# Optimization experiments

Measured on AMD Instinct MI355X. Metric: run time of the kernel, lower is better.

Reference implementation:

```python
import jax, jax.numpy as jnp
import numpy as np

N_NODES = 100000
N_EDGES = 1600000
N_GRAPHS = 256
NODE = 64
EDGE = 64
GLOB = 64
HID = 64


def _lin_init(key, fan_in, fan_out):
    kw, kb = jax.random.split(key)
    bound = 1.0 / np.sqrt(fan_in)
    W = jax.random.uniform(kw, (fan_in, fan_out), minval=-bound, maxval=bound, dtype=jnp.float32)
    b = jax.random.uniform(kb, (fan_out,), minval=-bound, maxval=bound, dtype=jnp.float32)
    return W, b


def setup_inputs() -> dict:
    key = jax.random.key(0)
    ks = jax.random.split(key, 9)
    x = jax.random.normal(ks[0], (N_NODES, NODE), dtype=jnp.float32)
    edge_index = jax.random.randint(ks[1], (2, N_EDGES), 0, N_NODES, dtype=jnp.int32)
    edge_attr = jax.random.normal(ks[2], (N_EDGES, EDGE), dtype=jnp.float32)
    u = jax.random.normal(ks[3], (N_GRAPHS, GLOB), dtype=jnp.float32)
    batch = jnp.sort(jax.random.randint(ks[4], (N_NODES,), 0, N_GRAPHS, dtype=jnp.int32))
    W1a, b1a = _lin_init(ks[5], NODE + EDGE, HID)
    W1b, b1b = _lin_init(ks[6], HID, HID)
    W2a, b2a = _lin_init(ks[7], NODE + HID + GLOB, HID)
    W2b, b2b = _lin_init(ks[8], HID, NODE)
    return {"x": x, "edge_index": edge_index, "edge_attr": edge_attr, "u": u,
            "batch": batch, "W1a": W1a, "b1a": b1a, "W1b": W1b, "b1b": b1b,
            "W2a": W2a, "b2a": b2a, "W2b": W2b, "b2b": b2b}


def reference(x, edge_index, edge_attr, u, batch, W1a, b1a, W1b, b1b, W2a, b2a, W2b, b2b):
    row, col = edge_index[0], edge_index[1]
    # gather source node feats + edge feats -> [E, node+edge]
    out = jnp.concatenate([x[row], edge_attr], axis=1)
    out = jax.nn.selu(out @ W1a + b1a) @ W1b + b1b  # node_mlp_1 -> [E, HID]
    # scatter_mean into destination nodes
    summed = jax.ops.segment_sum(out, col, num_segments=x.shape[0])
    counts = jax.ops.segment_sum(jnp.ones((out.shape[0],), out.dtype), col, num_segments=x.shape[0])
    mean = summed / jnp.maximum(counts, 1.0)[:, None]
    h = jnp.concatenate([x, mean, u[batch]], axis=1)  # [N, node+HID+glob]
    return jax.nn.selu(h @ W2a + b2a) @ W2b + b2b
```

## Files before the change

### kernel.cpp

```cpp
#include <hip/hip_runtime.h>

#define NN 100000
#define NE 1600000

typedef __attribute__((ext_vector_type(8))) short short8;
typedef __attribute__((ext_vector_type(4))) float f32x4;

__device__ __forceinline__ short f2b(float x) {
    unsigned u = __builtin_bit_cast(unsigned, x);
    u = (u + 0x7FFFu + ((u >> 16) & 1u)) >> 16;
    return (short)u;
}

__device__ __forceinline__ float selu_f(float x) {
    const float scale = 1.0507009873554805f;
    const float asc   = 1.7580993408473766f;
    return x > 0.f ? scale * x : asc * (__expf(x) - 1.f);
}

__device__ __forceinline__ short8 pack8(const float* __restrict__ p) {
    const float4 a = *reinterpret_cast<const float4*>(p);
    const float4 b = *reinterpret_cast<const float4*>(p + 4);
    short8 r;
    r[0] = f2b(a.x); r[1] = f2b(a.y); r[2] = f2b(a.z); r[3] = f2b(a.w);
    r[4] = f2b(b.x); r[5] = f2b(b.y); r[6] = f2b(b.z); r[7] = f2b(b.w);
    return r;
}

__device__ __forceinline__ short8 pack8s(const float* __restrict__ p, float s) {
    const float4 a = *reinterpret_cast<const float4*>(p);
    const float4 b = *reinterpret_cast<const float4*>(p + 4);
    short8 r;
    r[0] = f2b(a.x * s); r[1] = f2b(a.y * s); r[2] = f2b(a.z * s); r[3] = f2b(a.w * s);
    r[4] = f2b(b.x * s); r[5] = f2b(b.y * s); r[6] = f2b(b.z * s); r[7] = f2b(b.w * s);
    return r;
}

__device__ __forceinline__ short8 wfrag(const float* __restrict__ W, int t, int n, int p, int q) {
    const float* base = W + (t * 32 + q * 8) * 64 + n * 16 + p;
    short8 r;
#pragma unroll
    for (int j = 0; j < 8; ++j) r[j] = f2b(base[j * 64]);
    return r;
}

__device__ __forceinline__ f32x4 mm(short8 a, short8 b, f32x4 c) {
    return __builtin_amdgcn_mfma_f32_16x16x32_bf16(a, b, c, 0, 0, 0);
}

__global__ __launch_bounds__(256) void edge_kernel(
    const float* __restrict__ x, const int* __restrict__ row, const int* __restrict__ col,
    const float* __restrict__ ea,
    const float* __restrict__ W1a, const float* __restrict__ b1a,
    const float* __restrict__ W1b, const float* __restrict__ b1b,
    float* __restrict__ summed, float* __restrict__ counts)
{
    __shared__ __attribute__((aligned(16))) short hlds[4][16 * 72];
    const int lane = threadIdx.x & 63;
    const int wid  = threadIdx.x >> 6;
    const int p = lane & 15, q = lane >> 4;
    short* hl = hlds[wid];

    short8 B1[4][4], B2[2][4];
#pragma unroll
    for (int t = 0; t < 4; ++t)
#pragma unroll
        for (int n = 0; n < 4; ++n) B1[t][n] = wfrag(W1a, t, n, p, q);
#pragma unroll
    for (int t = 0; t < 2; ++t)
#pragma unroll
        for (int n = 0; n < 4; ++n) B2[t][n] = wfrag(W1b, t, n, p, q);
    float bias1[4], bias2[4];
#pragma unroll
    for (int n = 0; n < 4; ++n) { bias1[n] = b1a[n * 16 + p]; bias2[n] = b1b[n * 16 + p]; }

    const int nwave = gridDim.x * 4;
    for (int tile = blockIdx.x * 4 + wid; tile < NE / 16; tile += nwave) {
        const int e  = tile * 16 + p;
        const int rs = row[e];
        const float* xr = x + rs * 64 + q * 8;
        const float* er = ea + e * 64 + q * 8;
        short8 a0 = pack8(xr);
        short8 a1 = pack8(xr + 32);
        short8 a2 = pack8(er);
        short8 a3 = pack8(er + 32);

        f32x4 acc[4];
#pragma unroll
        for (int n = 0; n < 4; ++n) acc[n] = (f32x4){0.f, 0.f, 0.f, 0.f};
#pragma unroll
        for (int n = 0; n < 4; ++n) {
            acc[n] = mm(a0, B1[0][n], acc[n]);
            acc[n] = mm(a1, B1[1][n], acc[n]);
            acc[n] = mm(a2, B1[2][n], acc[n]);
            acc[n] = mm(a3, B1[3][n], acc[n]);
        }
#pragma unroll
        for (int n = 0; n < 4; ++n)
#pragma unroll
            for (int i = 0; i < 4; ++i)
                hl[(q * 4 + i) * 72 + n * 16 + p] = f2b(selu_f(acc[n][i] + bias1[n]));

        short8 h0 = *reinterpret_cast<const short8*>(hl + p * 72 + q * 8);
        short8 h1 = *reinterpret_cast<const short8*>(hl + p * 72 + 32 + q * 8);

        f32x4 acc2[4];
#pragma unroll
        for (int n = 0; n < 4; ++n) acc2[n] = (f32x4){0.f, 0.f, 0.f, 0.f};
#pragma unroll
        for (int n = 0; n < 4; ++n) {
            acc2[n] = mm(h0, B2[0][n], acc2[n]);
            acc2[n] = mm(h1, B2[1][n], acc2[n]);
        }

        int cd[4];
#pragma unroll
        for (int i = 0; i < 4; ++i) cd[i] = col[tile * 16 + q * 4 + i];
#pragma unroll
        for (int n = 0; n < 4; ++n)
#pragma unroll
            for (int i = 0; i < 4; ++i)
                unsafeAtomicAdd(&summed[cd[i] * 64 + n * 16 + p], acc2[n][i] + bias2[n]);
        if (lane < 16) unsafeAtomicAdd(&counts[col[e]], 1.0f);
    }
}

__global__ __launch_bounds__(256) void node_kernel(
    const float* __restrict__ x, const float* __restrict__ u, const int* __restrict__ batch,
    const float* __restrict__ summed, const float* __restrict__ counts,
    const float* __restrict__ W2a, const float* __restrict__ b2a,
    const float* __restrict__ W2b, const float* __restrict__ b2b,
    float* __restrict__ out)
{
    __shared__ __attribute__((aligned(16))) short hlds[4][16 * 72];
    const int lane = threadIdx.x & 63;
    const int wid  = threadIdx.x >> 6;
    const int p = lane & 15, q = lane >> 4;
    short* hl = hlds[wid];

    short8 BA[6][4], BB[2][4];
#pragma unroll
    for (int t = 0; t < 6; ++t)
#pragma unroll
        for (int n = 0; n < 4; ++n) BA[t][n] = wfrag(W2a, t, n, p, q);
#pragma unroll
    for (int t = 0; t < 2; ++t)
#pragma unroll
        for (int n = 0; n < 4; ++n) BB[t][n] = wfrag(W2b, t, n, p, q);
    float bias1[4], bias2[4];
#pragma unroll
    for (int n = 0; n < 4; ++n) { bias1[n] = b2a[n * 16 + p]; bias2[n] = b2b[n * 16 + p]; }

    const int nwave = gridDim.x * 4;
    for (int tile = blockIdx.x * 4 + wid; tile < NN / 16; tile += nwave) {
        const int v = tile * 16 + p;
        const float* xr = x + v * 64 + q * 8;
        short8 a0 = pack8(xr);
        short8 a1 = pack8(xr + 32);
        const float rc = 1.f / fmaxf(counts[v], 1.f);
        const float* sr = summed + v * 64 + q * 8;
        short8 a2 = pack8s(sr, rc);
        short8 a3 = pack8s(sr + 32, rc);
        const int g = batch[v];
        const float* ur = u + g * 64 + q * 8;
        short8 a4 = pack8(ur);
        short8 a5 = pack8(ur + 32);

        f32x4 acc[4];
#pragma unroll
        for (int n = 0; n < 4; ++n) acc[n] = (f32x4){0.f, 0.f, 0.f, 0.f};
#pragma unroll
        for (int n = 0; n < 4; ++n) {
            acc[n] = mm(a0, BA[0][n], acc[n]);
            acc[n] = mm(a1, BA[1][n], acc[n]);
            acc[n] = mm(a2, BA[2][n], acc[n]);
            acc[n] = mm(a3, BA[3][n], acc[n]);
            acc[n] = mm(a4, BA[4][n], acc[n]);
            acc[n] = mm(a5, BA[5][n], acc[n]);
        }
#pragma unroll
        for (int n = 0; n < 4; ++n)
#pragma unroll
            for (int i = 0; i < 4; ++i)
                hl[(q * 4 + i) * 72 + n * 16 + p] = f2b(selu_f(acc[n][i] + bias1[n]));

        short8 h0 = *reinterpret_cast<const short8*>(hl + p * 72 + q * 8);
        short8 h1 = *reinterpret_cast<const short8*>(hl + p * 72 + 32 + q * 8);

        f32x4 acc2[4];
#pragma unroll
        for (int n = 0; n < 4; ++n) acc2[n] = (f32x4){0.f, 0.f, 0.f, 0.f};
#pragma unroll
        for (int n = 0; n < 4; ++n) {
            acc2[n] = mm(h0, BB[0][n], acc2[n]);
            acc2[n] = mm(h1, BB[1][n], acc2[n]);
        }
#pragma unroll
        for (int n = 0; n < 4; ++n)
#pragma unroll
            for (int i = 0; i < 4; ++i)
                out[(tile * 16 + q * 4 + i) * 64 + n * 16 + p] = acc2[n][i] + bias2[n];
    }
}

extern "C" void kernel_launch(void* const* d_in, const int* in_sizes, int n_in,
                              void* d_out, int out_size, void* d_ws, size_t ws_size,
                              hipStream_t stream) {
    const float* x     = (const float*)d_in[0];
    const int*   ei    = (const int*)d_in[1];
    const float* ea    = (const float*)d_in[2];
    const float* u     = (const float*)d_in[3];
    const int*   batch = (const int*)d_in[4];
    const float* W1a   = (const float*)d_in[5];
    const float* b1a   = (const float*)d_in[6];
    const float* W1b   = (const float*)d_in[7];
    const float* b1b   = (const float*)d_in[8];
    const float* W2a   = (const float*)d_in[9];
    const float* b2a   = (const float*)d_in[10];
    const float* W2b   = (const float*)d_in[11];
    const float* b2b   = (const float*)d_in[12];
    float* out = (float*)d_out;

    float* summed = (float*)d_ws;
    float* counts = summed + (size_t)NN * 64;

    hipMemsetAsync(d_ws, 0, ((size_t)NN * 64 + NN) * sizeof(float), stream);

    const int* row = ei;
    const int* col = ei + NE;
    edge_kernel<<<1024, 256, 0, stream>>>(x, row, col, ea, W1a, b1a, W1b, b1b, summed, counts);
    node_kernel<<<512, 256, 0, stream>>>(x, u, batch, summed, counts, W2a, b2a, W2b, b2b, out);
}
```

Baseline: 882.5 us.

## Accumulate edge scatter in bf16 with packed atomics and prepack weight fragments

Stores the per-node sum buffer as bf16 and scatters edge messages with global_atomic_pk_add_bf16, pairing neighbouring lanes through a shuffle. This halves atomic traffic and the size of the buffer to clear. Weight fragments are converted to bf16 MFMA layout once by a small setup kernel instead of strided per-wave loads. The change also prefetches the next row index, uses nontemporal loads for edge_attr and doubles the node kernel grid. Summing up to many bf16 additions per node loses precision and may exceed tolerance.

```diff
diff --git a/kernel.cpp b/kernel.cpp
--- a/kernel.cpp
+++ b/kernel.cpp
@@ -2,6 +2,8 @@
 
 #define NN 100000
 #define NE 1600000
+#define NT_E (NE / 16)
+#define NT_N ((NN + 15) / 16)
 
 typedef __attribute__((ext_vector_type(8))) short short8;
 typedef __attribute__((ext_vector_type(4))) float f32x4;
@@ -11,6 +13,9 @@
     u = (u + 0x7FFFu + ((u >> 16) & 1u)) >> 16;
     return (short)u;
 }
+__device__ __forceinline__ float b2f(unsigned short b) {
+    return __builtin_bit_cast(float, (unsigned)b << 16);
+}
 
 __device__ __forceinline__ float selu_f(float x) {
     const float scale = 1.0507009873554805f;
@@ -19,41 +24,55 @@
 }
 
 __device__ __forceinline__ short8 pack8(const float* __restrict__ p) {
-    const float4 a = *reinterpret_cast<const float4*>(p);
-    const float4 b = *reinterpret_cast<const float4*>(p + 4);
+    const f32x4 a = *reinterpret_cast<const f32x4*>(p);
+    const f32x4 b = *reinterpret_cast<const f32x4*>(p + 4);
     short8 r;
-    r[0] = f2b(a.x); r[1] = f2b(a.y); r[2] = f2b(a.z); r[3] = f2b(a.w);
-    r[4] = f2b(b.x); r[5] = f2b(b.y); r[6] = f2b(b.z); r[7] = f2b(b.w);
+#pragma unroll
+    for (int j = 0; j < 4; ++j) { r[j] = f2b(a[j]); r[j + 4] = f2b(b[j]); }
     return r;
 }
 
-__device__ __forceinline__ short8 pack8s(const float* __restrict__ p, float s) {
-    const float4 a = *reinterpret_cast<const float4*>(p);
-    const float4 b = *reinterpret_cast<const float4*>(p + 4);
+__device__ __forceinline__ short8 pack8nt(const float* __restrict__ p) {
+    const f32x4 a = __builtin_nontemporal_load(reinterpret_cast<const f32x4*>(p));
+    const f32x4 b = __builtin_nontemporal_load(reinterpret_cast<const f32x4*>(p + 4));
     short8 r;
-    r[0] = f2b(a.x * s); r[1] = f2b(a.y * s); r[2] = f2b(a.z * s); r[3] = f2b(a.w * s);
-    r[4] = f2b(b.x * s); r[5] = f2b(b.y * s); r[6] = f2b(b.z * s); r[7] = f2b(b.w * s);
+#pragma unroll
+    for (int j = 0; j < 4; ++j) { r[j] = f2b(a[j]); r[j + 4] = f2b(b[j]); }
     return r;
 }
 
-__device__ __forceinline__ short8 wfrag(const float* __restrict__ W, int t, int n, int p, int q) {
-    const float* base = W + (t * 32 + q * 8) * 64 + n * 16 + p;
-    short8 r;
-#pragma unroll
-    for (int j = 0; j < 8; ++j) r[j] = f2b(base[j * 64]);
-    return r;
+__device__ __forceinline__ short8 ld_frag(const unsigned short* __restrict__ base, int idx, int lane) {
+    return *reinterpret_cast<const short8*>(base + ((size_t)idx * 64 + lane) * 8);
 }
 
 __device__ __forceinline__ f32x4 mm(short8 a, short8 b, f32x4 c) {
     return __builtin_amdgcn_mfma_f32_16x16x32_bf16(a, b, c, 0, 0, 0);
+}
+
+__global__ void frag_setup(const float* __restrict__ W1a, const float* __restrict__ W1b,
+                           const float* __restrict__ W2a, const float* __restrict__ W2b,
+                           unsigned short* __restrict__ fw) {
+    const int lane = threadIdx.x;
+    const int p = lane & 15, q = lane >> 4;
+    const int f = blockIdx.x;
+    const float* W; int idx; unsigned short* dst;
+    if (f < 16)      { W = W1a; idx = f;      dst = fw; }
+    else if (f < 24) { W = W1b; idx = f - 16; dst = fw + 16 * 512; }
+    else if (f < 48) { W = W2a; idx = f - 24; dst = fw + 24 * 512; }
+    else             { W = W2b; idx = f - 48; dst = fw + 48 * 512; }
+    const int t = idx >> 2, n = idx & 3;
+    const float* base = W + (t * 32 + q * 8) * 64 + n * 16 + p;
+    unsigned short* o = dst + ((size_t)idx * 64 + lane) * 8;
+#pragma unroll
+    for (int j = 0; j < 8; ++j) o[j] = (unsigned short)f2b(base[j * 64]);
 }
 
 __global__ __launch_bounds__(256) void edge_kernel(
     const float* __restrict__ x, const int* __restrict__ row, const int* __restrict__ col,
     const float* __restrict__ ea,
-    const float* __restrict__ W1a, const float* __restrict__ b1a,
-    const float* __restrict__ W1b, const float* __restrict__ b1b,
-    float* __restrict__ summed, float* __restrict__ counts)
+    const unsigned short* __restrict__ fw1a, const float* __restrict__ b1a,
+    const unsigned short* __restrict__ fw1b, const float* __restrict__ b1b,
+    unsigned short* __restrict__ summed, float* __restrict__ counts)
 {
     __shared__ __attribute__((aligned(16))) short hlds[4][16 * 72];
     const int lane = threadIdx.x & 63;
@@ -65,25 +84,34 @@
 #pragma unroll
     for (int t = 0; t < 4; ++t)
 #pragma unroll
-        for (int n = 0; n < 4; ++n) B1[t][n] = wfrag(W1a, t, n, p, q);
+        for (int n = 0; n < 4; ++n) B1[t][n] = ld_frag(fw1a, t * 4 + n, lane);
 #pragma unroll
     for (int t = 0; t < 2; ++t)
 #pragma unroll
-        for (int n = 0; n < 4; ++n) B2[t][n] = wfrag(W1b, t, n, p, q);
+        for (int n = 0; n < 4; ++n) B2[t][n] = ld_frag(fw1b, t * 4 + n, lane);
     float bias1[4], bias2[4];
 #pragma unroll
     for (int n = 0; n < 4; ++n) { bias1[n] = b1a[n * 16 + p]; bias2[n] = b1b[n * 16 + p]; }
 
-    const int nwave = gridDim.x * 4;
-    for (int tile = blockIdx.x * 4 + wid; tile < NE / 16; tile += nwave) {
-        const int e  = tile * 16 + p;
-        const int rs = row[e];
-        const float* xr = x + rs * 64 + q * 8;
-        const float* er = ea + e * 64 + q * 8;
+    const int tstride = gridDim.x * 4;
+    int tile = blockIdx.x * 4 + wid;
+    int rs = (tile < NT_E) ? row[tile * 16 + p] : 0;
+
+    for (; tile < NT_E; tile += tstride) {
+        const int e = tile * 16 + p;
+        const float* xr = x + (size_t)rs * 64 + q * 8;
+        const float* er = ea + (size_t)e * 64 + q * 8;
         short8 a0 = pack8(xr);
         short8 a1 = pack8(xr + 32);
-        short8 a2 = pack8(er);
-        short8 a3 = pack8(er + 32);
+        short8 a2 = pack8nt(er);
+        short8 a3 = pack8nt(er + 32);
+
+        const int tn = tile + tstride;
+        const int rs_next = (tn < NT_E) ? row[tn * 16 + p] : 0;
+
+        int cd[4];
+#pragma unroll
+        for (int i = 0; i < 4; ++i) cd[i] = col[tile * 16 + q * 4 + i];
 
         f32x4 acc[4];
 #pragma unroll
@@ -113,23 +141,31 @@
             acc2[n] = mm(h1, B2[1][n], acc2[n]);
         }
 
-        int cd[4];
-#pragma unroll
-        for (int i = 0; i < 4; ++i) cd[i] = col[tile * 16 + q * 4 + i];
-#pragma unroll
-        for (int n = 0; n < 4; ++n)
-#pragma unroll
-            for (int i = 0; i < 4; ++i)
-                unsafeAtomicAdd(&summed[cd[i] * 64 + n * 16 + p], acc2[n][i] + bias2[n]);
+#pragma unroll
+        for (int n = 0; n < 4; ++n)
+#pragma unroll
+            for (int i = 0; i < 4; ++i) {
+                const float v = acc2[n][i] + bias2[n];
+                const float o = __shfl_xor(v, 1);
+                if (!(p & 1)) {
+                    unsigned pk = ((unsigned)(unsigned short)f2b(o) << 16) |
+                                  (unsigned)(unsigned short)f2b(v);
+                    unsigned long long addr =
+                        (unsigned long long)(summed + (size_t)cd[i] * 64 + n * 16 + p);
+                    asm volatile("global_atomic_pk_add_bf16 %0, %1, off"
+                                 :: "v"(addr), "v"(pk) : "memory");
+                }
+            }
         if (lane < 16) unsafeAtomicAdd(&counts[col[e]], 1.0f);
+        rs = rs_next;
     }
 }
 
 __global__ __launch_bounds__(256) void node_kernel(
     const float* __restrict__ x, const float* __restrict__ u, const int* __restrict__ batch,
-    const float* __restrict__ summed, const float* __restrict__ counts,
-    const float* __restrict__ W2a, const float* __restrict__ b2a,
-    const float* __restrict__ W2b, const float* __restrict__ b2b,
+    const unsigned short* __restrict__ summed, const float* __restrict__ counts,
+    const unsigned short* __restrict__ fw2a, const float* __restrict__ b2a,
+    const unsigned short* __restrict__ fw2b, const float* __restrict__ b2b,
     float* __restrict__ out)
 {
     __shared__ __attribute__((aligned(16))) short hlds[4][16 * 72];
@@ -142,27 +178,34 @@
 #pragma unroll
     for (int t = 0; t < 6; ++t)
 #pragma unroll
-        for (int n = 0; n < 4; ++n) BA[t][n] = wfrag(W2a, t, n, p, q);
+        for (int n = 0; n < 4; ++n) BA[t][n] = ld_frag(fw2a, t * 4 + n, lane);
 #pragma unroll
     for (int t = 0; t < 2; ++t)
 #pragma unroll
-        for (int n = 0; n < 4; ++n) BB[t][n] = wfrag(W2b, t, n, p, q);
+        for (int n = 0; n < 4; ++n) BB[t][n] = ld_frag(fw2b, t * 4 + n, lane);
     float bias1[4], bias2[4];
 #pragma unroll
     for (int n = 0; n < 4; ++n) { bias1[n] = b2a[n * 16 + p]; bias2[n] = b2b[n * 16 + p]; }
 
-    const int nwave = gridDim.x * 4;
-    for (int tile = blockIdx.x * 4 + wid; tile < NN / 16; tile += nwave) {
+    const int tstride = gridDim.x * 4;
+    for (int tile = blockIdx.x * 4 + wid; tile < NT_N; tile += tstride) {
         const int v = tile * 16 + p;
-        const float* xr = x + v * 64 + q * 8;
+        const float* xr = x + (size_t)v * 64 + q * 8;
         short8 a0 = pack8(xr);
         short8 a1 = pack8(xr + 32);
+
         const float rc = 1.f / fmaxf(counts[v], 1.f);
-        const float* sr = summed + v * 64 + q * 8;
-        short8 a2 = pack8s(sr, rc);
-        short8 a3 = pack8s(sr + 32, rc);
+        const unsigned short* sr = summed + (size_t)v * 64 + q * 8;
+        short8 s0 = *reinterpret_cast<const short8*>(sr);
+        short8 s1 = *reinterpret_cast<const short8*>(sr + 32);
+        short8 a2, a3;
+#pragma unroll
+        for (int j = 0; j < 8; ++j) {
+            a2[j] = f2b(b2f((unsigned short)s0[j]) * rc);
+            a3[j] = f2b(b2f((unsigned short)s1[j]) * rc);
+        }
         const int g = batch[v];
-        const float* ur = u + g * 64 + q * 8;
+        const float* ur = u + (size_t)g * 64 + q * 8;
         short8 a4 = pack8(ur);
         short8 a5 = pack8(ur + 32);
 
@@ -199,7 +242,7 @@
         for (int n = 0; n < 4; ++n)
 #pragma unroll
             for (int i = 0; i < 4; ++i)
-                out[(tile * 16 + q * 4 + i) * 64 + n * 16 + p] = acc2[n][i] + bias2[n];
+                out[((size_t)tile * 16 + q * 4 + i) * 64 + n * 16 + p] = acc2[n][i] + bias2[n];
     }
 }
 
@@ -221,13 +264,19 @@
     const float* b2b   = (const float*)d_in[12];
     float* out = (float*)d_out;
 
-    float* summed = (float*)d_ws;
-    float* counts = summed + (size_t)NN * 64;
-
-    hipMemsetAsync(d_ws, 0, ((size_t)NN * 64 + NN) * sizeof(float), stream);
+    unsigned short* summed = (unsigned short*)d_ws;
+    float* counts = (float*)((char*)d_ws + (size_t)NN * 64 * 2);
+    unsigned short* fw = (unsigned short*)((char*)d_ws + 13200000);
+    const unsigned short* fw1a = fw;
+    const unsigned short* fw1b = fw + 16 * 512;
+    const unsigned short* fw2a = fw + 24 * 512;
+    const unsigned short* fw2b = fw + 48 * 512;
+
+    hipMemsetAsync(d_ws, 0, 13200000, stream);
+    frag_setup<<<56, 64, 0, stream>>>(W1a, W1b, W2a, W2b, fw);
 
     const int* row = ei;
     const int* col = ei + NE;
-    edge_kernel<<<1024, 256, 0, stream>>>(x, row, col, ea, W1a, b1a, W1b, b1b, summed, counts);
-    node_kernel<<<512, 256, 0, stream>>>(x, u, batch, summed, counts, W2a, b2a, W2b, b2b, out);
-}
+    edge_kernel<<<1024, 256, 0, stream>>>(x, row, col, ea, fw1a, b1a, fw1b, b1b, summed, counts);
+    node_kernel<<<1024, 256, 0, stream>>>(x, u, batch, summed, counts, fw2a, b2a, fw2b, b2b, out);
+}
```

After: 908.9 us. 3.0% more time.
